# Kernel tuning notes

Hardware: AMD Instinct MI355X
Metric: run time of the kernel (lower is better)

The kernel has to match this reference:

```python
import jax, jax.numpy as jnp
import numpy as np

NUM_CLASSES = 80
STRIDES = (8, 16, 32)
RADIUS = 2.5
BOX_WEIGHT = 5.0
BIG = 1e9  # emulates restriction of cost/matching to union-candidate anchors
CAND_K = 10


def setup_inputs() -> dict:
    key = jax.random.key(0)
    ks = jax.random.split(key, 6)
    B, G = 16, 16
    p0 = jax.random.normal(ks[0], (B, NUM_CLASSES + 5, 160, 160), jnp.float32)
    p1 = jax.random.normal(ks[1], (B, NUM_CLASSES + 5, 80, 80), jnp.float32)
    p2 = jax.random.normal(ks[2], (B, NUM_CLASSES + 5, 40, 40), jnp.float32)
    cxy = jax.random.uniform(ks[3], (B, G, 2), jnp.float32, 64.0, 1216.0)
    wh = jax.random.uniform(ks[4], (B, G, 2), jnp.float32, 16.0, 256.0)
    cls = jax.random.randint(ks[5], (B, G, 1), 0, NUM_CLASSES).astype(jnp.float32)
    labels = jnp.concatenate([cxy, wh, cls], axis=-1)  # [B,G,5] xywh + class id
    return {"p0": p0, "p1": p1, "p2": p2, "labels": labels}


def _decode(p, stride):
    # [B,C,H,W] -> [B,HW,C] with xy=(xy+grid)*stride, wh=exp(wh)*stride
    B, C, H, W = p.shape
    out = jnp.transpose(p.reshape(B, C, H * W), (0, 2, 1))
    yy, xx = jnp.meshgrid(jnp.arange(H, dtype=p.dtype), jnp.arange(W, dtype=p.dtype), indexing='ij')
    gx, gy = xx.reshape(-1), yy.reshape(-1)
    xy = (out[..., :2] + jnp.stack([gx, gy], axis=-1)) * stride
    wh = jnp.exp(out[..., 2:4]) * stride
    return jnp.concatenate([xy, wh, out[..., 4:]], axis=-1), gx, gy


def _pair_iou(a, b):
    # a:[G,4], b:[A,4] in xywh -> [G,A]
    a1, a2 = a[:, :2] - a[:, 2:] * 0.5, a[:, :2] + a[:, 2:] * 0.5
    b1, b2 = b[:, :2] - b[:, 2:] * 0.5, b[:, :2] + b[:, 2:] * 0.5
    tl = jnp.maximum(a1[:, None], b1[None])
    br = jnp.minimum(a2[:, None], b2[None])
    wh = jnp.maximum(br - tl, 0.0)
    inter = wh[..., 0] * wh[..., 1]
    return inter / (a[:, 2] * a[:, 3])[:, None].__add__((b[:, 2] * b[:, 3])[None]).__sub__(inter).__add__(1e-16)


def _elem_iou(a, b):
    # elementwise xywh iou on [...,4]
    a1, a2 = a[..., :2] - a[..., 2:] * 0.5, a[..., :2] + a[..., 2:] * 0.5
    b1, b2 = b[..., :2] - b[..., 2:] * 0.5, b[..., :2] + b[..., 2:] * 0.5
    wh = jnp.maximum(jnp.minimum(a2, b2) - jnp.maximum(a1, b1), 0.0)
    inter = wh[..., 0] * wh[..., 1]
    return inter / (a[..., 2] * a[..., 3] + b[..., 2] * b[..., 3] - inter + 1e-16)


def _bce_logits(x, t):
    return jnp.maximum(x, 0.0) - x * t + jnp.log1p(jnp.exp(-jnp.abs(x)))


def _assign(tb, tc, pbox, pcls_l, pconf_l, xc, yc, sv):
    # Per-image SimOTA. tb:[G,4] tc:[G] pbox:[A,4] pcls_l:[A,C] pconf_l:[A]
    G = tb.shape[0]
    bx, by, bw, bh = tb[:, 0:1], tb[:, 1:2], tb[:, 2:3], tb[:, 3:4]
    in_box = (xc[None] > bx - bw * 0.5) & (xc[None] < bx + bw * 0.5) & \
             (yc[None] > by - bh * 0.5) & (yc[None] < by + bh * 0.5)  # [G,A]
    r = RADIUS * sv[None]
    in_mir = (xc[None] > bx - r) & (xc[None] < bx + r) & (yc[None] > by - r) & (yc[None] < by + r)
    union = jnp.any(in_box, 0) | jnp.any(in_mir, 0)  # [A]
    inter = in_box & in_mir  # [G,A]
    iou = _pair_iou(tb, pbox)  # [G,A]
    # cls cost: BCE(sqrt(sigmoid(cls)*sigmoid(conf)), one_hot) summed over classes
    p = jnp.sqrt(jax.nn.sigmoid(pcls_l) * jax.nn.sigmoid(pconf_l)[:, None])  # [A,C]
    logp = jnp.clip(jnp.log(p), -100.0, None)
    log1mp = jnp.clip(jnp.log1p(-p), -100.0, None)
    base = -log1mp.sum(-1)  # [A] = sum_c -log(1-p)
    cls_cost = base[None] - logp[:, tc].T + log1mp[:, tc].T  # [G,A]
    cost = cls_cost - 3.0 * jnp.log(iou + 1e-8) + 1e5 * (~inter) + BIG * (~union)[None]
    iou_m = jnp.where(union[None], iou, 0.0)
    dyn_k = jnp.maximum(jax.lax.top_k(iou_m, CAND_K)[0].sum(1).astype(jnp.int32), 1)  # [G]
    _, idx = jax.lax.top_k(-cost, CAND_K)  # per-gt lowest-cost anchors, sorted
    sel = (jnp.arange(CAND_K)[None] < dyn_k[:, None]).astype(cost.dtype)  # [G,K]
    matching = jnp.zeros_like(cost).at[jnp.arange(G)[:, None], idx].max(sel)  # [G,A]
    conflict = matching.sum(0) > 1.0
    gt_min = jnp.argmin(cost, axis=0)  # [A]
    onehot_min = (jnp.arange(G)[:, None] == gt_min[None]).astype(cost.dtype)
    matching = jnp.where(conflict[None], onehot_min, matching)
    fg = matching.sum(0) > 0.0  # [A]
    gidx = jnp.argmax(matching, axis=0)  # [A]
    miou = (matching * iou).sum(0)  # [A]
    t_cls = jax.nn.one_hot(tc[gidx], NUM_CLASSES, dtype=cost.dtype) * miou[:, None]  # [A,C]
    t_box = tb[gidx]  # [A,4]
    return fg, t_cls, t_box


def _forward(p0, p1, p2, labels):
    outs, xcs, ycs, svs = [], [], [], []
    for p, s in zip((p0, p1, p2), STRIDES):
        o, gx, gy = _decode(p, float(s))
        outs.append(o)
        xcs.append((gx + 0.5) * s)
        ycs.append((gy + 0.5) * s)
        svs.append(jnp.full_like(gx, s))
    out = jnp.concatenate(outs, axis=1)  # [B,A,85]
    xc, yc, sv = jnp.concatenate(xcs), jnp.concatenate(ycs), jnp.concatenate(svs)
    pbox, pconf, pcls = out[..., :4], out[..., 4], out[..., 5:]
    tb, tc = labels[..., :4], labels[..., 4].astype(jnp.int32)
    assign = jax.vmap(_assign, in_axes=(0, 0, 0, 0, 0, None, None, None))
    fg, t_cls, t_box = jax.lax.stop_gradient(assign(tb, tc, pbox, pcls, pconf, xc, yc, sv))
    fgf = fg.astype(pbox.dtype)  # target_conf == final fg mask
    loss_box = (fgf * (1.0 - _elem_iou(pbox, t_box) ** 2)).sum()
    loss_conf = _bce_logits(pconf, fgf).sum()
    loss_cls = (fgf[..., None] * _bce_logits(pcls, t_cls)).sum()
    fg_num = jnp.maximum(fgf.sum(), 1.0)
    return (BOX_WEIGHT * loss_box + loss_conf + loss_cls) / fg_num


def reference(p0, p1, p2, labels):
    return _forward(p0, p1, p2, labels)
```

## Files before the change

kernel.cpp:

```cpp
#include <hip/hip_runtime.h>
#include <hip/hip_bf16.h>
#include <cstdint>

#define NCLS 80
#define GNUM 16
#define BNUM 16
#define A0   25600
#define A1   6400
#define A2   1600
#define ATOT 33600
#define QTOT 16800
#define NBLK_A 132
#define NBLK_TOTAL (NBLK_A*BNUM)
#define NSPLIT 8
#define SEG   4200
#define WSEG  1050
#define NWAVE 32
#define FINF  3.4e38f
#define IINF  0x7fffffff

__device__ __forceinline__ float rcpf(float x){ return __builtin_amdgcn_rcpf(x); }
__device__ __forceinline__ float sqf (float x){ return __builtin_amdgcn_sqrtf(x); }
__device__ __forceinline__ float rsqf(float x){ return __builtin_amdgcn_rsqf(x); }

__device__ __forceinline__ float bce(float x, float t){
  float e = __expf(-fabsf(x));
  return fmaxf(x,0.f) - x*t + __logf(1.f + e);
}

__device__ __forceinline__ void get_level(const float* p0, const float* p1, const float* p2,
                                          int a, const float*& p, int& hw, int& off, int& W, float& s)
{
  if (a < A0){ p=p0; hw=A0; off=a; W=160; s=8.f; }
  else if (a < A0+A1){ p=p1; hw=A1; off=a-A0; W=80; s=16.f; }
  else { p=p2; hw=A2; off=a-A0-A1; W=40; s=32.f; }
}

__global__ __launch_bounds__(256, 8) void decode_cost_kernel(
    const float* __restrict__ p0, const float* __restrict__ p1, const float* __restrict__ p2,
    const float* __restrict__ labels,
    float* __restrict__ cost, float4* __restrict__ pbox, float* __restrict__ pconf,
    unsigned char* __restrict__ unionm)
{
  const int b = blockIdx.y;
  const int t = threadIdx.x;
  __shared__ float s_tb[GNUM][4];
  __shared__ int   s_tc[GNUM];
  if (t < GNUM){
    const float* L = labels + ((size_t)b*GNUM + t)*5;
    s_tb[t][0]=L[0]; s_tb[t][1]=L[1]; s_tb[t][2]=L[2]; s_tb[t][3]=L[3];
    s_tc[t]=(int)L[4];
  }
  __syncthreads();
  const int q = blockIdx.x*64 + (t>>2);
  const int k = t & 3;
  if (q >= QTOT) return;
  const int a0 = q*2;

  const float* p; int hw, off, W; float s;
  get_level(p0,p1,p2,a0,p,hw,off,W,s);
  const float* bp = p + (size_t)b*(NCLS+5)*hw + off;
  const float* cp = bp + 5*(size_t)hw;

  const float2 RX = *(const float2*)(bp);
  const float2 RY = *(const float2*)(bp + (size_t)hw);
  const float2 RW = *(const float2*)(bp + 2*(size_t)hw);
  const float2 RH = *(const float2*)(bp + 3*(size_t)hw);
  const float2 CL = *(const float2*)(bp + 4*(size_t)hw);

  int gx0 = off % W, gy0 = off / W;
  int gx1 = gx0+1, gy1 = gy0; if (gx1 >= W){ gx1 = 0; gy1++; }

  const float sc0 = rcpf(1.f + __expf(-CL.x));
  const float sc1 = rcpf(1.f + __expf(-CL.y));
  const float ssc0 = sqf(sc0),   ssc1 = sqf(sc1);
  const float rssc0 = rcpf(ssc0), rssc1 = rcpf(ssc1);

  float part0 = 0.f, part1 = 0.f;
  const int cb = 20*k;
  {
    float2 xv[8];
    #pragma unroll
    for (int j=0;j<8;j++) xv[j] = *(const float2*)(cp + (size_t)(cb+j)*hw);
    float pr0=1.f, pr1=1.f;
    #pragma unroll
    for (int j=0;j<8;j++){
      pr0 *= (1.f - ssc0*rsqf(1.f+__expf(-xv[j].x)));
      pr1 *= (1.f - ssc1*rsqf(1.f+__expf(-xv[j].y)));
    }
    part0 -= __logf(pr0); part1 -= __logf(pr1);
  }
  {
    float2 xv[8];
    #pragma unroll
    for (int j=0;j<8;j++) xv[j] = *(const float2*)(cp + (size_t)(cb+8+j)*hw);
    float pr0=1.f, pr1=1.f;
    #pragma unroll
    for (int j=0;j<8;j++){
      pr0 *= (1.f - ssc0*rsqf(1.f+__expf(-xv[j].x)));
      pr1 *= (1.f - ssc1*rsqf(1.f+__expf(-xv[j].y)));
    }
    part0 -= __logf(pr0); part1 -= __logf(pr1);
  }
  {
    float2 xv[4];
    #pragma unroll
    for (int j=0;j<4;j++) xv[j] = *(const float2*)(cp + (size_t)(cb+16+j)*hw);
    float pr0=1.f, pr1=1.f;
    #pragma unroll
    for (int j=0;j<4;j++){
      pr0 *= (1.f - ssc0*rsqf(1.f+__expf(-xv[j].x)));
      pr1 *= (1.f - ssc1*rsqf(1.f+__expf(-xv[j].y)));
    }
    part0 -= __logf(pr0); part1 -= __logf(pr1);
  }
  float base0 = part0 + __shfl_xor(part0, 1); base0 += __shfl_xor(base0, 2);
  float base1 = part1 + __shfl_xor(part1, 1); base1 += __shfl_xor(base1, 2);

  const float px0=(RX.x+gx0)*s, py0=(RY.x+gy0)*s, pw0=__expf(RW.x)*s, ph0=__expf(RH.x)*s;
  const float px1=(RX.y+gx1)*s, py1=(RY.y+gy1)*s, pw1=__expf(RW.y)*s, ph1=__expf(RH.y)*s;
  const float xc0=(gx0+0.5f)*s, yc0=(gy0+0.5f)*s;
  const float xc1=(gx1+0.5f)*s, yc1=(gy1+0.5f)*s;
  const float q1x0=px0-pw0*0.5f, q2x0=px0+pw0*0.5f, q1y0=py0-ph0*0.5f, q2y0=py0+ph0*0.5f;
  const float q1x1=px1-pw1*0.5f, q2x1=px1+pw1*0.5f, q1y1=py1-ph1*0.5f, q2y1=py1+ph1*0.5f;
  const float areaP0 = pw0*ph0, areaP1 = pw1*ph1;
  const float r = 2.5f*s;

  int mybits = 0;
  #pragma unroll
  for (int j=0;j<4;j++){
    const int g = k*4 + j;
    const float bx=s_tb[g][0], by=s_tb[g][1], bw=s_tb[g][2], bh=s_tb[g][3];
    const float b1x=bx-bw*0.5f, b2x=bx+bw*0.5f, b1y=by-bh*0.5f, b2y=by+bh*0.5f;
    const bool u0 = ((xc0>b1x)&&(xc0<b2x)&&(yc0>b1y)&&(yc0<b2y))
                  || ((xc0>bx-r)&&(xc0<bx+r)&&(yc0>by-r)&&(yc0<by+r));
    const bool u1 = ((xc1>b1x)&&(xc1<b2x)&&(yc1>b1y)&&(yc1<b2y))
                  || ((xc1>bx-r)&&(xc1<bx+r)&&(yc1>by-r)&&(yc1<by+r));
    mybits |= (u0?1:0) | (u1?2:0);
  }
  mybits |= __shfl_xor(mybits, 1);
  mybits |= __shfl_xor(mybits, 2);
  const float add0 = (mybits&1)?0.f:1e9f, add1 = (mybits&2)?0.f:1e9f;

  const size_t rowb = (size_t)b*GNUM*ATOT + a0;

  #pragma unroll
  for (int j=0;j<4;j++){
    const int g = k*4 + j;
    const float2 x = *(const float2*)(cp + (size_t)s_tc[g]*hw);
    const float e0 = __expf(-x.x), e1 = __expf(-x.y);
    const float rp0 = rssc0*sqf(1.f+e0), rp1 = rssc1*sqf(1.f+e1);
    const float cd0 = __logf(fmaxf(rp0-1.f, 1e-30f));
    const float cd1 = __logf(fmaxf(rp1-1.f, 1e-30f));

    const float bx=s_tb[g][0], by=s_tb[g][1], bw=s_tb[g][2], bh=s_tb[g][3];
    const float b1x=bx-bw*0.5f, b2x=bx+bw*0.5f, b1y=by-bh*0.5f, b2y=by+bh*0.5f;
    const float areaB = bw*bh;

    const bool inb0 = (xc0>b1x)&&(xc0<b2x)&&(yc0>b1y)&&(yc0<b2y);
    const bool inm0 = (xc0>bx-r)&&(xc0<bx+r)&&(yc0>by-r)&&(yc0<by+r);
    const bool inb1 = (xc1>b1x)&&(xc1<b2x)&&(yc1>b1y)&&(yc1<b2y);
    const bool inm1 = (xc1>bx-r)&&(xc1<bx+r)&&(yc1>by-r)&&(yc1<by+r);

    float iw,ih,inte;
    iw = fmaxf(fminf(b2x,q2x0)-fmaxf(b1x,q1x0),0.f);
    ih = fmaxf(fminf(b2y,q2y0)-fmaxf(b1y,q1y0),0.f);
    inte = iw*ih;
    const float iou0 = inte * rcpf(areaB+areaP0-inte+1e-16f);
    iw = fmaxf(fminf(b2x,q2x1)-fmaxf(b1x,q1x1),0.f);
    ih = fmaxf(fminf(b2y,q2y1)-fmaxf(b1y,q1y1),0.f);
    inte = iw*ih;
    const float iou1 = inte * rcpf(areaB+areaP1-inte+1e-16f);

    float2 cst;
    cst.x = base0 + cd0 - 3.f*__logf(iou0+1e-8f) + ((inb0&&inm0)?0.f:100000.f) + add0;
    cst.y = base1 + cd1 - 3.f*__logf(iou1+1e-8f) + ((inb1&&inm1)?0.f:100000.f) + add1;
    *(float2*)(cost + rowb + (size_t)g*ATOT) = cst;
  }

  if (k == 0){
    pbox[(size_t)b*ATOT+a0  ] = make_float4(px0,py0,pw0,ph0);
    pbox[(size_t)b*ATOT+a0+1] = make_float4(px1,py1,pw1,ph1);
    *(float2*)(pconf + (size_t)b*ATOT + a0) = make_float2(CL.x, CL.y);
    uchar2 um; um.x = (mybits&1)?1:0; um.y = (mybits&2)?1:0;
    *(uchar2*)(unionm + (size_t)b*ATOT + a0) = um;
  }
}

__global__ __launch_bounds__(256) void topk_stage1(
    const float* __restrict__ cost, const float4* __restrict__ pbox,
    const unsigned char* __restrict__ unionm, const float* __restrict__ labels,
    float* __restrict__ cand_c, int* __restrict__ cand_i, float* __restrict__ cand_v)
{
  const int bg   = blockIdx.y;
  const int b    = bg >> 4;
  const int seg  = blockIdx.x;
  const int wave = threadIdx.x >> 6;
  const int lane = threadIdx.x & 63;
  const int wg   = seg*4 + wave;

  const float*  crow = cost + (size_t)bg*ATOT;
  const float4* prow = pbox + (size_t)b*ATOT;
  const unsigned char* urow = unionm + (size_t)b*ATOT;
  const float bx = labels[bg*5+0], by = labels[bg*5+1];
  const float bw = labels[bg*5+2], bh = labels[bg*5+3];
  const float areaB = bw*bh;
  const float b1x=bx-bw*0.5f, b2x=bx+bw*0.5f, b1y=by-bh*0.5f, b2y=by+bh*0.5f;

  const int start = seg*SEG + wave*WSEG;
  const int end   = start + WSEG;

  float cv[10]; int ci[10]; float iv[10];
  #pragma unroll
  for (int k=0;k<10;k++){ cv[k]=FINF; ci[k]=IINF; iv[k]=0.f; }

  for (int a = start + lane; a < end; a += 64){
    float c = crow[a];
    if (c < cv[9] || (c == cv[9] && a < ci[9])){
      float nc=c; int ni=a;
      #pragma unroll
      for (int k=0;k<10;k++){
        bool better = (nc < cv[k]) || (nc==cv[k] && ni<ci[k]);
        float tv=cv[k]; int ti=ci[k];
        cv[k]=better?nc:cv[k]; ci[k]=better?ni:ci[k];
        nc  =better?tv:nc;     ni  =better?ti:ni;
      }
    }
    if (urow[a]){
      float4 pb = prow[a];
      float tlx=fmaxf(b1x, pb.x-pb.z*0.5f), brx=fminf(b2x, pb.x+pb.z*0.5f);
      float tly=fmaxf(b1y, pb.y-pb.w*0.5f), bry=fminf(b2y, pb.y+pb.w*0.5f);
      float iw=fmaxf(brx-tlx,0.f), ih=fmaxf(bry-tly,0.f);
      float inte=iw*ih;
      float io = inte * rcpf(areaB + pb.z*pb.w - inte + 1e-16f);
      if (io > iv[9]){
        float nv=io;
        #pragma unroll
        for (int k=0;k<10;k++){
          bool better = nv > iv[k];
          float tv=iv[k];
          iv[k]=better?nv:iv[k];
          nv  =better?tv:nv;
        }
      }
    }
  }

  float selc = 0.f; int seli = 0;
  #pragma unroll
  for (int r=0;r<10;r++){
    float bv = cv[0]; int bi = ci[0];
    #pragma unroll
    for (int off=32; off>0; off>>=1){
      float ov = __shfl_xor(bv, off);
      int   oi = __shfl_xor(bi, off);
      bool take = (ov < bv) || (ov==bv && oi<bi);
      bv = take?ov:bv; bi = take?oi:bi;
    }
    if (lane == r){ selc = bv; seli = bi; }
    if (cv[0]==bv && ci[0]==bi){
      #pragma unroll
      for (int k=0;k<9;k++){ cv[k]=cv[k+1]; ci[k]=ci[k+1]; }
      cv[9]=FINF; ci[9]=IINF;
    }
  }
  float selv = 0.f;
  #pragma unroll
  for (int r=0;r<10;r++){
    float bv = iv[0]; int bl = lane;
    #pragma unroll
    for (int off=32; off>0; off>>=1){
      float ov = __shfl_xor(bv, off);
      int   ol = __shfl_xor(bl, off);
      bool take = (ov > bv) || (ov==bv && ol<bl);
      bv = take?ov:bv; bl = take?ol:bl;
    }
    if (lane == r) selv = bv;
    if (lane == bl){
      #pragma unroll
      for (int k=0;k<9;k++){ iv[k]=iv[k+1]; }
      iv[9]=0.f;
    }
  }

  if (lane < 10){
    const size_t base = ((size_t)bg*NWAVE + wg)*10 + lane;
    cand_c[base] = selc;
    cand_i[base] = seli;
    cand_v[base] = selv;
  }
}

__global__ __launch_bounds__(64) void topk_stage2(
    const float* __restrict__ cand_c, const int* __restrict__ cand_i,
    const float* __restrict__ cand_v, unsigned int* __restrict__ match_mask)
{
  const int bg = blockIdx.x;
  const int b = bg >> 4, g = bg & 15;
  const int lane = threadIdx.x;
  const size_t base = (size_t)bg*NWAVE*10 + lane*5;

  float cv[5]; int ci[5]; float iv[5];
  #pragma unroll
  for (int k=0;k<5;k++){ cv[k]=cand_c[base+k]; ci[k]=cand_i[base+k]; iv[k]=cand_v[base+k]; }

  int seli = 0;
  #pragma unroll
  for (int r=0;r<10;r++){
    float bv = cv[0]; int bi = ci[0];
    #pragma unroll
    for (int off=32; off>0; off>>=1){
      float ov = __shfl_xor(bv, off);
      int   oi = __shfl_xor(bi, off);
      bool take = (ov < bv) || (ov==bv && oi<bi);
      bv = take?ov:bv; bi = take?oi:bi;
    }
    if (lane == r) seli = bi;
    if (cv[0]==bv && ci[0]==bi){
      #pragma unroll
      for (int k=0;k<4;k++){ cv[k]=cv[k+1]; ci[k]=ci[k+1]; }
      cv[4]=FINF; ci[4]=IINF;
    }
  }

  float isum = 0.f;
  #pragma unroll
  for (int r=0;r<10;r++){
    float bv = iv[0]; int bl = lane;
    #pragma unroll
    for (int off=32; off>0; off>>=1){
      float ov = __shfl_xor(bv, off);
      int   ol = __shfl_xor(bl, off);
      bool take = (ov > bv) || (ov==bv && ol<bl);
      bv = take?ov:bv; bl = take?ol:bl;
    }
    isum += bv;
    if (lane == bl){
      #pragma unroll
      for (int k=0;k<4;k++){ iv[k]=iv[k+1]; }
      iv[4]=0.f;
    }
  }

  int dynk = (int)isum;
  if (dynk < 1)  dynk = 1;
  if (dynk > 10) dynk = 10;
  if (lane < dynk)
    atomicOr(&match_mask[(size_t)b*ATOT + seli], 1u<<g);
}

__global__ __launch_bounds__(256) void loss_kernel(
    const float* __restrict__ p0, const float* __restrict__ p1, const float* __restrict__ p2,
    const float* __restrict__ labels,
    const float* __restrict__ cost, const float4* __restrict__ pbox,
    const float* __restrict__ pconf, const unsigned int* __restrict__ match_mask,
    float* __restrict__ blocksums)
{
  const int b = blockIdx.y;
  const int a = blockIdx.x*256 + threadIdx.x;
  float lbox=0.f, lconf=0.f, lcls=0.f, fgn=0.f;
  if (a < ATOT){
    unsigned int m = match_mask[(size_t)b*ATOT+a];
    float cl = pconf[(size_t)b*ATOT+a];
    if (m != 0u){
      int gidx;
      if (__popc(m) > 1){
        float best = FINF; int bgi = 0;
        for (int g=0; g<GNUM; g++){
          float c = cost[((size_t)b*GNUM+g)*ATOT + a];
          if (c < best){ best=c; bgi=g; }
        }
        gidx = bgi;
      } else {
        gidx = __ffs(m)-1;
      }
      const float* L = labels + ((size_t)b*GNUM+gidx)*5;
      float bx=L[0], by=L[1], bw=L[2], bh=L[3];
      int tcg=(int)L[4];
      float4 pb = pbox[(size_t)b*ATOT+a];
      float tlx=fmaxf(bx-bw*0.5f, pb.x-pb.z*0.5f);
      float brx=fminf(bx+bw*0.5f, pb.x+pb.z*0.5f);
      float tly=fmaxf(by-bh*0.5f, pb.y-pb.w*0.5f);
      float bry=fminf(by+bh*0.5f, pb.y+pb.w*0.5f);
      float iw=fmaxf(brx-tlx,0.f), ih=fmaxf(bry-tly,0.f);
      float inte=iw*ih;
      float iou = inte * rcpf(bw*bh + pb.z*pb.w - inte + 1e-16f);
      lbox = 1.f - iou*iou;
      lconf = bce(cl, 1.f);
      float miou = iou;
      const float* p; int hw, off, W; float s;
      get_level(p0,p1,p2,a,p,hw,off,W,s);
      const float* bp = p + (size_t)b*(NCLS+5)*hw + off;
      for (int c=0;c<NCLS;c++){
        float x = bp[(size_t)(5+c)*hw];
        float t = (c==tcg)? miou : 0.f;
        lcls += bce(x, t);
      }
      fgn = 1.f;
    } else {
      lconf = bce(cl, 0.f);
    }
  }
  #pragma unroll
  for (int off2=32; off2>0; off2>>=1){
    lbox  += __shfl_down(lbox,  off2);
    lconf += __shfl_down(lconf, off2);
    lcls  += __shfl_down(lcls,  off2);
    fgn   += __shfl_down(fgn,   off2);
  }
  __shared__ float s_red[4][4];
  const int wave = threadIdx.x >> 6;
  if ((threadIdx.x & 63)==0){
    s_red[wave][0]=lbox; s_red[wave][1]=lconf; s_red[wave][2]=lcls; s_red[wave][3]=fgn;
  }
  __syncthreads();
  if (threadIdx.x==0){
    float r0=0,r1=0,r2=0,r3=0;
    #pragma unroll
    for (int w=0;w<4;w++){ r0+=s_red[w][0]; r1+=s_red[w][1]; r2+=s_red[w][2]; r3+=s_red[w][3]; }
    const int bid = blockIdx.y*gridDim.x + blockIdx.x;
    ((float4*)blocksums)[bid] = make_float4(r0,r1,r2,r3);
  }
}

__global__ __launch_bounds__(256) void finalize_kernel(
    const float* __restrict__ blocksums, float* __restrict__ out)
{
  const int tid = threadIdx.x;
  float r0=0,r1=0,r2=0,r3=0;
  for (int i = tid; i < NBLK_TOTAL; i += 256){
    const float4 v = ((const float4*)blocksums)[i];
    r0+=v.x; r1+=v.y; r2+=v.z; r3+=v.w;
  }
  #pragma unroll
  for (int off=32; off>0; off>>=1){
    r0 += __shfl_down(r0, off);
    r1 += __shfl_down(r1, off);
    r2 += __shfl_down(r2, off);
    r3 += __shfl_down(r3, off);
  }
  __shared__ float s_red[4][4];
  const int wave = tid >> 6;
  if ((tid & 63)==0){ s_red[wave][0]=r0; s_red[wave][1]=r1; s_red[wave][2]=r2; s_red[wave][3]=r3; }
  __syncthreads();
  if (tid==0){
    float t0=0,t1=0,t2=0,t3=0;
    #pragma unroll
    for (int w=0;w<4;w++){ t0+=s_red[w][0]; t1+=s_red[w][1]; t2+=s_red[w][2]; t3+=s_red[w][3]; }
    out[0] = (5.f*t0 + t1 + t2) / fmaxf(t3, 1.f);
  }
}

extern "C" void kernel_launch(void* const* d_in, const int* in_sizes, int n_in,
                              void* d_out, int out_size, void* d_ws, size_t ws_size,
                              hipStream_t stream)
{
  const float* p0     = (const float*)d_in[0];
  const float* p1     = (const float*)d_in[1];
  const float* p2     = (const float*)d_in[2];
  const float* labels = (const float*)d_in[3];

  char* ws = (char*)d_ws;
  size_t o = 0;
  float*        cost       = (float*)(ws + o);        o += (size_t)BNUM*GNUM*ATOT*4;
  float4*       pbox       = (float4*)(ws + o);       o += (size_t)BNUM*ATOT*16;
  float*        pconf      = (float*)(ws + o);        o += (size_t)BNUM*ATOT*4;
  unsigned int* match_mask = (unsigned int*)(ws + o); o += (size_t)BNUM*ATOT*4;
  unsigned char* unionm    = (unsigned char*)(ws + o);o += (size_t)BNUM*ATOT;
  o = (o + 255) & ~(size_t)255;
  float*        blocksums  = (float*)(ws + o);        o += (size_t)NBLK_TOTAL*4*4;
  o = (o + 255) & ~(size_t)255;
  float*        cand_c     = (float*)(ws + o);        o += (size_t)256*NWAVE*10*4;
  int*          cand_i     = (int*)(ws + o);          o += (size_t)256*NWAVE*10*4;
  float*        cand_v     = (float*)(ws + o);        o += (size_t)256*NWAVE*10*4;

  hipMemsetAsync(match_mask, 0, (size_t)BNUM*ATOT*4, stream);

  dim3 gridA((QTOT + 63)/64, BNUM);
  decode_cost_kernel<<<gridA, 256, 0, stream>>>(p0,p1,p2,labels,cost,pbox,pconf,unionm);
  dim3 gridT(NSPLIT, BNUM*GNUM);
  topk_stage1<<<gridT, 256, 0, stream>>>(cost, pbox, unionm, labels, cand_c, cand_i, cand_v);
  topk_stage2<<<BNUM*GNUM, 64, 0, stream>>>(cand_c, cand_i, cand_v, match_mask);
  dim3 gridC(NBLK_A, BNUM);
  loss_kernel<<<gridC, 256, 0, stream>>>(p0,p1,p2,labels,cost,pbox,pconf,match_mask,blocksums);
  finalize_kernel<<<1, 256, 0, stream>>>(blocksums, (float*)d_out);
}
```

Baseline: 142.7 us.

## Fuse per-block top-k into decode kernel and drop global cost matrix

The decode kernel now keeps each block's 16x128 cost and IoU tiles in shared memory and does a wave-level top-10 selection there, writing only small candidate lists instead of the full B*G*A cost matrix. A merge kernel reduces these candidates, and the loss kernel recomputes cost for multi-matched anchors instead of reading the stored matrix. This removes roughly 34 MB of cost writes and reads and the separate memset, since match_mask is zeroed inside the decode kernel. In exchange it adds in-kernel reduction work, extra shared memory (lower occupancy), and redundant class reads for conflicting anchors.

```diff
diff --git a/kernel.cpp b/kernel.cpp
--- a/kernel.cpp
+++ b/kernel.cpp
@@ -12,9 +12,9 @@
 #define QTOT 16800
 #define NBLK_A 132
 #define NBLK_TOTAL (NBLK_A*BNUM)
-#define NSPLIT 8
-#define SEG   4200
-#define WSEG  1050
+#define NSEG 263
+#define NC   (NSEG*10)
+#define CHUNK 83
 #define NWAVE 32
 #define FINF  3.4e38f
 #define IINF  0x7fffffff
@@ -39,185 +39,237 @@
 __global__ __launch_bounds__(256, 8) void decode_cost_kernel(
     const float* __restrict__ p0, const float* __restrict__ p1, const float* __restrict__ p2,
     const float* __restrict__ labels,
-    float* __restrict__ cost, float4* __restrict__ pbox, float* __restrict__ pconf,
-    unsigned char* __restrict__ unionm)
+    float4* __restrict__ pbox, float* __restrict__ pconf,
+    unsigned char* __restrict__ unionm, unsigned int* __restrict__ match_mask,
+    float* __restrict__ cand1_c, int* __restrict__ cand1_i, float* __restrict__ cand1_v)
 {
   const int b = blockIdx.y;
   const int t = threadIdx.x;
   __shared__ float s_tb[GNUM][4];
   __shared__ int   s_tc[GNUM];
+  __shared__ float s_cost[GNUM][128];
+  __shared__ float s_iou [GNUM][128];
   if (t < GNUM){
     const float* L = labels + ((size_t)b*GNUM + t)*5;
     s_tb[t][0]=L[0]; s_tb[t][1]=L[1]; s_tb[t][2]=L[2]; s_tb[t][3]=L[3];
     s_tc[t]=(int)L[4];
   }
   __syncthreads();
-  const int q = blockIdx.x*64 + (t>>2);
+  const int p_loc = t>>2;
+  const int q = blockIdx.x*64 + p_loc;
   const int k = t & 3;
-  if (q >= QTOT) return;
-  const int a0 = q*2;
-
-  const float* p; int hw, off, W; float s;
-  get_level(p0,p1,p2,a0,p,hw,off,W,s);
-  const float* bp = p + (size_t)b*(NCLS+5)*hw + off;
-  const float* cp = bp + 5*(size_t)hw;
-
-  const float2 RX = *(const float2*)(bp);
-  const float2 RY = *(const float2*)(bp + (size_t)hw);
-  const float2 RW = *(const float2*)(bp + 2*(size_t)hw);
-  const float2 RH = *(const float2*)(bp + 3*(size_t)hw);
-  const float2 CL = *(const float2*)(bp + 4*(size_t)hw);
-
-  int gx0 = off % W, gy0 = off / W;
-  int gx1 = gx0+1, gy1 = gy0; if (gx1 >= W){ gx1 = 0; gy1++; }
-
-  const float sc0 = rcpf(1.f + __expf(-CL.x));
-  const float sc1 = rcpf(1.f + __expf(-CL.y));
-  const float ssc0 = sqf(sc0),   ssc1 = sqf(sc1);
-  const float rssc0 = rcpf(ssc0), rssc1 = rcpf(ssc1);
-
-  float part0 = 0.f, part1 = 0.f;
-  const int cb = 20*k;
-  {
-    float2 xv[8];
-    #pragma unroll
-    for (int j=0;j<8;j++) xv[j] = *(const float2*)(cp + (size_t)(cb+j)*hw);
-    float pr0=1.f, pr1=1.f;
-    #pragma unroll
-    for (int j=0;j<8;j++){
-      pr0 *= (1.f - ssc0*rsqf(1.f+__expf(-xv[j].x)));
-      pr1 *= (1.f - ssc1*rsqf(1.f+__expf(-xv[j].y)));
-    }
-    part0 -= __logf(pr0); part1 -= __logf(pr1);
-  }
-  {
-    float2 xv[8];
-    #pragma unroll
-    for (int j=0;j<8;j++) xv[j] = *(const float2*)(cp + (size_t)(cb+8+j)*hw);
-    float pr0=1.f, pr1=1.f;
-    #pragma unroll
-    for (int j=0;j<8;j++){
-      pr0 *= (1.f - ssc0*rsqf(1.f+__expf(-xv[j].x)));
-      pr1 *= (1.f - ssc1*rsqf(1.f+__expf(-xv[j].y)));
-    }
-    part0 -= __logf(pr0); part1 -= __logf(pr1);
-  }
-  {
-    float2 xv[4];
-    #pragma unroll
-    for (int j=0;j<4;j++) xv[j] = *(const float2*)(cp + (size_t)(cb+16+j)*hw);
-    float pr0=1.f, pr1=1.f;
+  const bool valid = (q < QTOT);
+
+  if (!valid){
     #pragma unroll
     for (int j=0;j<4;j++){
-      pr0 *= (1.f - ssc0*rsqf(1.f+__expf(-xv[j].x)));
-      pr1 *= (1.f - ssc1*rsqf(1.f+__expf(-xv[j].y)));
-    }
-    part0 -= __logf(pr0); part1 -= __logf(pr1);
-  }
-  float base0 = part0 + __shfl_xor(part0, 1); base0 += __shfl_xor(base0, 2);
-  float base1 = part1 + __shfl_xor(part1, 1); base1 += __shfl_xor(base1, 2);
-
-  const float px0=(RX.x+gx0)*s, py0=(RY.x+gy0)*s, pw0=__expf(RW.x)*s, ph0=__expf(RH.x)*s;
-  const float px1=(RX.y+gx1)*s, py1=(RY.y+gy1)*s, pw1=__expf(RW.y)*s, ph1=__expf(RH.y)*s;
-  const float xc0=(gx0+0.5f)*s, yc0=(gy0+0.5f)*s;
-  const float xc1=(gx1+0.5f)*s, yc1=(gy1+0.5f)*s;
-  const float q1x0=px0-pw0*0.5f, q2x0=px0+pw0*0.5f, q1y0=py0-ph0*0.5f, q2y0=py0+ph0*0.5f;
-  const float q1x1=px1-pw1*0.5f, q2x1=px1+pw1*0.5f, q1y1=py1-ph1*0.5f, q2y1=py1+ph1*0.5f;
-  const float areaP0 = pw0*ph0, areaP1 = pw1*ph1;
-  const float r = 2.5f*s;
-
-  int mybits = 0;
-  #pragma unroll
-  for (int j=0;j<4;j++){
-    const int g = k*4 + j;
-    const float bx=s_tb[g][0], by=s_tb[g][1], bw=s_tb[g][2], bh=s_tb[g][3];
-    const float b1x=bx-bw*0.5f, b2x=bx+bw*0.5f, b1y=by-bh*0.5f, b2y=by+bh*0.5f;
-    const bool u0 = ((xc0>b1x)&&(xc0<b2x)&&(yc0>b1y)&&(yc0<b2y))
-                  || ((xc0>bx-r)&&(xc0<bx+r)&&(yc0>by-r)&&(yc0<by+r));
-    const bool u1 = ((xc1>b1x)&&(xc1<b2x)&&(yc1>b1y)&&(yc1<b2y))
-                  || ((xc1>bx-r)&&(xc1<bx+r)&&(yc1>by-r)&&(yc1<by+r));
-    mybits |= (u0?1:0) | (u1?2:0);
-  }
-  mybits |= __shfl_xor(mybits, 1);
-  mybits |= __shfl_xor(mybits, 2);
-  const float add0 = (mybits&1)?0.f:1e9f, add1 = (mybits&2)?0.f:1e9f;
-
-  const size_t rowb = (size_t)b*GNUM*ATOT + a0;
-
-  #pragma unroll
-  for (int j=0;j<4;j++){
-    const int g = k*4 + j;
-    const float2 x = *(const float2*)(cp + (size_t)s_tc[g]*hw);
-    const float e0 = __expf(-x.x), e1 = __expf(-x.y);
-    const float rp0 = rssc0*sqf(1.f+e0), rp1 = rssc1*sqf(1.f+e1);
-    const float cd0 = __logf(fmaxf(rp0-1.f, 1e-30f));
-    const float cd1 = __logf(fmaxf(rp1-1.f, 1e-30f));
-
-    const float bx=s_tb[g][0], by=s_tb[g][1], bw=s_tb[g][2], bh=s_tb[g][3];
-    const float b1x=bx-bw*0.5f, b2x=bx+bw*0.5f, b1y=by-bh*0.5f, b2y=by+bh*0.5f;
-    const float areaB = bw*bh;
-
-    const bool inb0 = (xc0>b1x)&&(xc0<b2x)&&(yc0>b1y)&&(yc0<b2y);
-    const bool inm0 = (xc0>bx-r)&&(xc0<bx+r)&&(yc0>by-r)&&(yc0<by+r);
-    const bool inb1 = (xc1>b1x)&&(xc1<b2x)&&(yc1>b1y)&&(yc1<b2y);
-    const bool inm1 = (xc1>bx-r)&&(xc1<bx+r)&&(yc1>by-r)&&(yc1<by+r);
-
-    float iw,ih,inte;
-    iw = fmaxf(fminf(b2x,q2x0)-fmaxf(b1x,q1x0),0.f);
-    ih = fmaxf(fminf(b2y,q2y0)-fmaxf(b1y,q1y0),0.f);
-    inte = iw*ih;
-    const float iou0 = inte * rcpf(areaB+areaP0-inte+1e-16f);
-    iw = fmaxf(fminf(b2x,q2x1)-fmaxf(b1x,q1x1),0.f);
-    ih = fmaxf(fminf(b2y,q2y1)-fmaxf(b1y,q1y1),0.f);
-    inte = iw*ih;
-    const float iou1 = inte * rcpf(areaB+areaP1-inte+1e-16f);
-
-    float2 cst;
-    cst.x = base0 + cd0 - 3.f*__logf(iou0+1e-8f) + ((inb0&&inm0)?0.f:100000.f) + add0;
-    cst.y = base1 + cd1 - 3.f*__logf(iou1+1e-8f) + ((inb1&&inm1)?0.f:100000.f) + add1;
-    *(float2*)(cost + rowb + (size_t)g*ATOT) = cst;
-  }
-
-  if (k == 0){
-    pbox[(size_t)b*ATOT+a0  ] = make_float4(px0,py0,pw0,ph0);
-    pbox[(size_t)b*ATOT+a0+1] = make_float4(px1,py1,pw1,ph1);
-    *(float2*)(pconf + (size_t)b*ATOT + a0) = make_float2(CL.x, CL.y);
-    uchar2 um; um.x = (mybits&1)?1:0; um.y = (mybits&2)?1:0;
-    *(uchar2*)(unionm + (size_t)b*ATOT + a0) = um;
-  }
-}
-
-__global__ __launch_bounds__(256) void topk_stage1(
-    const float* __restrict__ cost, const float4* __restrict__ pbox,
-    const unsigned char* __restrict__ unionm, const float* __restrict__ labels,
+      const int g = k*4 + j;
+      s_cost[g][2*p_loc]   = FINF;  s_cost[g][2*p_loc+1] = FINF;
+      s_iou [g][2*p_loc]   = 0.f;   s_iou [g][2*p_loc+1] = 0.f;
+    }
+  } else {
+    const int a0 = q*2;
+    const float* p; int hw, off, W; float s;
+    get_level(p0,p1,p2,a0,p,hw,off,W,s);
+    const float* bp = p + (size_t)b*(NCLS+5)*hw + off;
+    const float* cp = bp + 5*(size_t)hw;
+
+    const float2 RX = *(const float2*)(bp);
+    const float2 RY = *(const float2*)(bp + (size_t)hw);
+    const float2 RW = *(const float2*)(bp + 2*(size_t)hw);
+    const float2 RH = *(const float2*)(bp + 3*(size_t)hw);
+    const float2 CL = *(const float2*)(bp + 4*(size_t)hw);
+
+    int gx0 = off % W, gy0 = off / W;
+    int gx1 = gx0+1, gy1 = gy0; if (gx1 >= W){ gx1 = 0; gy1++; }
+
+    const float sc0 = rcpf(1.f + __expf(-CL.x));
+    const float sc1 = rcpf(1.f + __expf(-CL.y));
+    const float ssc0 = sqf(sc0),   ssc1 = sqf(sc1);
+    const float rssc0 = rcpf(ssc0), rssc1 = rcpf(ssc1);
+
+    float part0 = 0.f, part1 = 0.f;
+    const int cb = 20*k;
+    {
+      float2 xv[8];
+      #pragma unroll
+      for (int j=0;j<8;j++) xv[j] = *(const float2*)(cp + (size_t)(cb+j)*hw);
+      float pr0=1.f, pr1=1.f;
+      #pragma unroll
+      for (int j=0;j<8;j++){
+        pr0 *= (1.f - ssc0*rsqf(1.f+__expf(-xv[j].x)));
+        pr1 *= (1.f - ssc1*rsqf(1.f+__expf(-xv[j].y)));
+      }
+      part0 -= __logf(pr0); part1 -= __logf(pr1);
+    }
+    {
+      float2 xv[8];
+      #pragma unroll
+      for (int j=0;j<8;j++) xv[j] = *(const float2*)(cp + (size_t)(cb+8+j)*hw);
+      float pr0=1.f, pr1=1.f;
+      #pragma unroll
+      for (int j=0;j<8;j++){
+        pr0 *= (1.f - ssc0*rsqf(1.f+__expf(-xv[j].x)));
+        pr1 *= (1.f - ssc1*rsqf(1.f+__expf(-xv[j].y)));
+      }
+      part0 -= __logf(pr0); part1 -= __logf(pr1);
+    }
+    {
+      float2 xv[4];
+      #pragma unroll
+      for (int j=0;j<4;j++) xv[j] = *(const float2*)(cp + (size_t)(cb+16+j)*hw);
+      float pr0=1.f, pr1=1.f;
+      #pragma unroll
+      for (int j=0;j<4;j++){
+        pr0 *= (1.f - ssc0*rsqf(1.f+__expf(-xv[j].x)));
+        pr1 *= (1.f - ssc1*rsqf(1.f+__expf(-xv[j].y)));
+      }
+      part0 -= __logf(pr0); part1 -= __logf(pr1);
+    }
+    float base0 = part0 + __shfl_xor(part0, 1); base0 += __shfl_xor(base0, 2);
+    float base1 = part1 + __shfl_xor(part1, 1); base1 += __shfl_xor(base1, 2);
+
+    const float px0=(RX.x+gx0)*s, py0=(RY.x+gy0)*s, pw0=__expf(RW.x)*s, ph0=__expf(RH.x)*s;
+    const float px1=(RX.y+gx1)*s, py1=(RY.y+gy1)*s, pw1=__expf(RW.y)*s, ph1=__expf(RH.y)*s;
+    const float xc0=(gx0+0.5f)*s, yc0=(gy0+0.5f)*s;
+    const float xc1=(gx1+0.5f)*s, yc1=(gy1+0.5f)*s;
+    const float q1x0=px0-pw0*0.5f, q2x0=px0+pw0*0.5f, q1y0=py0-ph0*0.5f, q2y0=py0+ph0*0.5f;
+    const float q1x1=px1-pw1*0.5f, q2x1=px1+pw1*0.5f, q1y1=py1-ph1*0.5f, q2y1=py1+ph1*0.5f;
+    const float areaP0 = pw0*ph0, areaP1 = pw1*ph1;
+    const float r = 2.5f*s;
+
+    int mybits = 0;
+    #pragma unroll
+    for (int j=0;j<4;j++){
+      const int g = k*4 + j;
+      const float bx=s_tb[g][0], by=s_tb[g][1], bw=s_tb[g][2], bh=s_tb[g][3];
+      const float b1x=bx-bw*0.5f, b2x=bx+bw*0.5f, b1y=by-bh*0.5f, b2y=by+bh*0.5f;
+      const bool u0 = ((xc0>b1x)&&(xc0<b2x)&&(yc0>b1y)&&(yc0<b2y))
+                    || ((xc0>bx-r)&&(xc0<bx+r)&&(yc0>by-r)&&(yc0<by+r));
+      const bool u1 = ((xc1>b1x)&&(xc1<b2x)&&(yc1>b1y)&&(yc1<b2y))
+                    || ((xc1>bx-r)&&(xc1<bx+r)&&(yc1>by-r)&&(yc1<by+r));
+      mybits |= (u0?1:0) | (u1?2:0);
+    }
+    mybits |= __shfl_xor(mybits, 1);
+    mybits |= __shfl_xor(mybits, 2);
+    const float add0 = (mybits&1)?0.f:1e9f, add1 = (mybits&2)?0.f:1e9f;
+
+    #pragma unroll
+    for (int j=0;j<4;j++){
+      const int g = k*4 + j;
+      const float2 x = *(const float2*)(cp + (size_t)s_tc[g]*hw);
+      const float e0 = __expf(-x.x), e1 = __expf(-x.y);
+      const float rp0 = rssc0*sqf(1.f+e0), rp1 = rssc1*sqf(1.f+e1);
+      const float cd0 = __logf(fmaxf(rp0-1.f, 1e-30f));
+      const float cd1 = __logf(fmaxf(rp1-1.f, 1e-30f));
+
+      const float bx=s_tb[g][0], by=s_tb[g][1], bw=s_tb[g][2], bh=s_tb[g][3];
+      const float b1x=bx-bw*0.5f, b2x=bx+bw*0.5f, b1y=by-bh*0.5f, b2y=by+bh*0.5f;
+      const float areaB = bw*bh;
+
+      const bool inb0 = (xc0>b1x)&&(xc0<b2x)&&(yc0>b1y)&&(yc0<b2y);
+      const bool inm0 = (xc0>bx-r)&&(xc0<bx+r)&&(yc0>by-r)&&(yc0<by+r);
+      const bool inb1 = (xc1>b1x)&&(xc1<b2x)&&(yc1>b1y)&&(yc1<b2y);
+      const bool inm1 = (xc1>bx-r)&&(xc1<bx+r)&&(yc1>by-r)&&(yc1<by+r);
+
+      float iw,ih,inte;
+      iw = fmaxf(fminf(b2x,q2x0)-fmaxf(b1x,q1x0),0.f);
+      ih = fmaxf(fminf(b2y,q2y0)-fmaxf(b1y,q1y0),0.f);
+      inte = iw*ih;
+      const float iou0 = inte * rcpf(areaB+areaP0-inte+1e-16f);
+      iw = fmaxf(fminf(b2x,q2x1)-fmaxf(b1x,q1x1),0.f);
+      ih = fmaxf(fminf(b2y,q2y1)-fmaxf(b1y,q1y1),0.f);
+      inte = iw*ih;
+      const float iou1 = inte * rcpf(areaB+areaP1-inte+1e-16f);
+
+      s_cost[g][2*p_loc]   = base0 + cd0 - 3.f*__logf(iou0+1e-8f) + ((inb0&&inm0)?0.f:100000.f) + add0;
+      s_cost[g][2*p_loc+1] = base1 + cd1 - 3.f*__logf(iou1+1e-8f) + ((inb1&&inm1)?0.f:100000.f) + add1;
+      s_iou [g][2*p_loc]   = (mybits&1)? iou0 : 0.f;
+      s_iou [g][2*p_loc+1] = (mybits&2)? iou1 : 0.f;
+    }
+
+    if (k == 0){
+      const int a0w = q*2;
+      pbox[(size_t)b*ATOT+a0w  ] = make_float4(px0,py0,pw0,ph0);
+      pbox[(size_t)b*ATOT+a0w+1] = make_float4(px1,py1,pw1,ph1);
+      *(float2*)(pconf + (size_t)b*ATOT + a0w) = make_float2(CL.x, CL.y);
+      uchar2 um; um.x = (mybits&1)?1:0; um.y = (mybits&2)?1:0;
+      *(uchar2*)(unionm + (size_t)b*ATOT + a0w) = um;
+      uint2 z; z.x=0u; z.y=0u;
+      *(uint2*)(match_mask + (size_t)b*ATOT + a0w) = z;
+    }
+  }
+  __syncthreads();
+
+  const int wave = t>>6, lane = t&63;
+  #pragma unroll
+  for (int gg=0; gg<4; gg++){
+    const int g = wave*4 + gg;
+    const size_t cbase = ((size_t)(b*GNUM+g)*NSEG + blockIdx.x)*10;
+
+    float c0 = s_cost[g][lane],    c1 = s_cost[g][lane+64];
+    int   i0 = blockIdx.x*128+lane, i1 = blockIdx.x*128+lane+64;
+    {
+      bool sw = (c1 < c0) || (c1==c0 && i1 < i0);
+      float tc=c0; int ti=i0;
+      c0 = sw?c1:c0; i0 = sw?i1:i0;
+      c1 = sw?tc:c1; i1 = sw?ti:i1;
+    }
+    float selc=0.f; int seli=0;
+    #pragma unroll
+    for (int r2=0;r2<10;r2++){
+      float bv=c0; int bi=i0;
+      #pragma unroll
+      for (int off=32; off>0; off>>=1){
+        float ov=__shfl_xor(bv,off); int oi=__shfl_xor(bi,off);
+        bool take=(ov<bv)||(ov==bv&&oi<bi);
+        bv=take?ov:bv; bi=take?oi:bi;
+      }
+      if (lane==r2){ selc=bv; seli=bi; }
+      if (c0==bv && i0==bi){ c0=c1; i0=i1; c1=FINF; i1=IINF; }
+    }
+    if (lane<10){ cand1_c[cbase+lane]=selc; cand1_i[cbase+lane]=seli; }
+
+    float v0 = s_iou[g][lane], v1 = s_iou[g][lane+64];
+    if (v1 > v0){ float tv=v0; v0=v1; v1=tv; }
+    float selv=0.f;
+    #pragma unroll
+    for (int r2=0;r2<10;r2++){
+      float bv=v0; int bl=lane;
+      #pragma unroll
+      for (int off=32; off>0; off>>=1){
+        float ov=__shfl_xor(bv,off); int ol=__shfl_xor(bl,off);
+        bool take=(ov>bv)||(ov==bv&&ol<bl);
+        bv=take?ov:bv; bl=take?ol:bl;
+      }
+      if (lane==r2) selv=bv;
+      if (lane==bl){ v0=v1; v1=0.f; }
+    }
+    if (lane<10) cand1_v[cbase+lane]=selv;
+  }
+}
+
+__global__ __launch_bounds__(256) void topk_merge1(
+    const float* __restrict__ cand1_c, const int* __restrict__ cand1_i,
+    const float* __restrict__ cand1_v,
     float* __restrict__ cand_c, int* __restrict__ cand_i, float* __restrict__ cand_v)
 {
   const int bg   = blockIdx.y;
-  const int b    = bg >> 4;
-  const int seg  = blockIdx.x;
   const int wave = threadIdx.x >> 6;
   const int lane = threadIdx.x & 63;
-  const int wg   = seg*4 + wave;
-
-  const float*  crow = cost + (size_t)bg*ATOT;
-  const float4* prow = pbox + (size_t)b*ATOT;
-  const unsigned char* urow = unionm + (size_t)b*ATOT;
-  const float bx = labels[bg*5+0], by = labels[bg*5+1];
-  const float bw = labels[bg*5+2], bh = labels[bg*5+3];
-  const float areaB = bw*bh;
-  const float b1x=bx-bw*0.5f, b2x=bx+bw*0.5f, b1y=by-bh*0.5f, b2y=by+bh*0.5f;
-
-  const int start = seg*SEG + wave*WSEG;
-  const int end   = start + WSEG;
+  const int wg   = blockIdx.x*4 + wave;
+  const size_t base1 = (size_t)bg*NC;
+  const int start = wg*CHUNK;
+  const int end   = (start+CHUNK < NC)? start+CHUNK : NC;
 
   float cv[10]; int ci[10]; float iv[10];
   #pragma unroll
   for (int k=0;k<10;k++){ cv[k]=FINF; ci[k]=IINF; iv[k]=0.f; }
 
-  for (int a = start + lane; a < end; a += 64){
-    float c = crow[a];
-    if (c < cv[9] || (c == cv[9] && a < ci[9])){
-      float nc=c; int ni=a;
+  for (int c = start + lane; c < end; c += 64){
+    float cc = cand1_c[base1+c]; int ii = cand1_i[base1+c];
+    if (cc < cv[9] || (cc == cv[9] && ii < ci[9])){
+      float nc=cc; int ni=ii;
       #pragma unroll
       for (int k=0;k<10;k++){
         bool better = (nc < cv[k]) || (nc==cv[k] && ni<ci[k]);
@@ -226,22 +278,15 @@
         nc  =better?tv:nc;     ni  =better?ti:ni;
       }
     }
-    if (urow[a]){
-      float4 pb = prow[a];
-      float tlx=fmaxf(b1x, pb.x-pb.z*0.5f), brx=fminf(b2x, pb.x+pb.z*0.5f);
-      float tly=fmaxf(b1y, pb.y-pb.w*0.5f), bry=fminf(b2y, pb.y+pb.w*0.5f);
-      float iw=fmaxf(brx-tlx,0.f), ih=fmaxf(bry-tly,0.f);
-      float inte=iw*ih;
-      float io = inte * rcpf(areaB + pb.z*pb.w - inte + 1e-16f);
-      if (io > iv[9]){
-        float nv=io;
-        #pragma unroll
-        for (int k=0;k<10;k++){
-          bool better = nv > iv[k];
-          float tv=iv[k];
-          iv[k]=better?nv:iv[k];
-          nv  =better?tv:nv;
-        }
+    float vv = cand1_v[base1+c];
+    if (vv > iv[9]){
+      float nv=vv;
+      #pragma unroll
+      for (int k=0;k<10;k++){
+        bool better = nv > iv[k];
+        float tv=iv[k];
+        iv[k]=better?nv:iv[k];
+        nv  =better?tv:nv;
       }
     }
   }
@@ -352,8 +397,8 @@
 __global__ __launch_bounds__(256) void loss_kernel(
     const float* __restrict__ p0, const float* __restrict__ p1, const float* __restrict__ p2,
     const float* __restrict__ labels,
-    const float* __restrict__ cost, const float4* __restrict__ pbox,
-    const float* __restrict__ pconf, const unsigned int* __restrict__ match_mask,
+    const float4* __restrict__ pbox, const float* __restrict__ pconf,
+    const unsigned char* __restrict__ unionm, const unsigned int* __restrict__ match_mask,
     float* __restrict__ blocksums)
 {
   const int b = blockIdx.y;
@@ -363,12 +408,60 @@
     unsigned int m = match_mask[(size_t)b*ATOT+a];
     float cl = pconf[(size_t)b*ATOT+a];
     if (m != 0u){
+      const float* p; int hw, off, W; float s;
+      get_level(p0,p1,p2,a,p,hw,off,W,s);
+      const float* bp = p + (size_t)b*(NCLS+5)*hw + off;
+      const float* cp = bp + 5*(size_t)hw;
       int gidx;
       if (__popc(m) > 1){
+        float sc = rcpf(1.f + __expf(-cl));
+        float ssc = sqf(sc); float rssc = rcpf(ssc);
+        float part[4];
+        #pragma unroll
+        for (int kk=0; kk<4; kk++){
+          const int cb2 = 20*kk;
+          float pk = 0.f, pr;
+          pr = 1.f;
+          #pragma unroll
+          for (int j=0;j<8;j++)  pr *= (1.f - ssc*rsqf(1.f+__expf(-cp[(size_t)(cb2+j)*hw])));
+          pk -= __logf(pr);
+          pr = 1.f;
+          #pragma unroll
+          for (int j=8;j<16;j++) pr *= (1.f - ssc*rsqf(1.f+__expf(-cp[(size_t)(cb2+j)*hw])));
+          pk -= __logf(pr);
+          pr = 1.f;
+          #pragma unroll
+          for (int j=16;j<20;j++)pr *= (1.f - ssc*rsqf(1.f+__expf(-cp[(size_t)(cb2+j)*hw])));
+          pk -= __logf(pr);
+          part[kk] = pk;
+        }
+        const float base = (part[0]+part[1])+(part[2]+part[3]);
+        const int gx = off % W, gy = off / W;
+        const float xc=(gx+0.5f)*s, yc=(gy+0.5f)*s, r=2.5f*s;
+        const float4 pb = pbox[(size_t)b*ATOT+a];
+        const float q1x=pb.x-pb.z*0.5f, q2x=pb.x+pb.z*0.5f;
+        const float q1y=pb.y-pb.w*0.5f, q2y=pb.y+pb.w*0.5f;
+        const float areaP = pb.z*pb.w;
+        const float addu = unionm[(size_t)b*ATOT+a] ? 0.f : 1e9f;
         float best = FINF; int bgi = 0;
         for (int g=0; g<GNUM; g++){
-          float c = cost[((size_t)b*GNUM+g)*ATOT + a];
-          if (c < best){ best=c; bgi=g; }
+          const float* L = labels + ((size_t)b*GNUM+g)*5;
+          const float bx=L[0], by=L[1], bw=L[2], bh=L[3];
+          const int tc=(int)L[4];
+          const float x = cp[(size_t)tc*hw];
+          const float e = __expf(-x);
+          const float rp = rssc*sqf(1.f+e);
+          const float cd = __logf(fmaxf(rp-1.f, 1e-30f));
+          const float b1x=bx-bw*0.5f, b2x=bx+bw*0.5f, b1y=by-bh*0.5f, b2y=by+bh*0.5f;
+          const float areaB = bw*bh;
+          const bool inb = (xc>b1x)&&(xc<b2x)&&(yc>b1y)&&(yc<b2y);
+          const bool inm = (xc>bx-r)&&(xc<bx+r)&&(yc>by-r)&&(yc<by+r);
+          float iw = fmaxf(fminf(b2x,q2x)-fmaxf(b1x,q1x),0.f);
+          float ih = fmaxf(fminf(b2y,q2y)-fmaxf(b1y,q1y),0.f);
+          float inte = iw*ih;
+          const float iou = inte * rcpf(areaB+areaP-inte+1e-16f);
+          const float cg = base + cd - 3.f*__logf(iou+1e-8f) + ((inb&&inm)?0.f:100000.f) + addu;
+          if (cg < best){ best=cg; bgi=g; }
         }
         gidx = bgi;
       } else {
@@ -388,11 +481,8 @@
       lbox = 1.f - iou*iou;
       lconf = bce(cl, 1.f);
       float miou = iou;
-      const float* p; int hw, off, W; float s;
-      get_level(p0,p1,p2,a,p,hw,off,W,s);
-      const float* bp = p + (size_t)b*(NCLS+5)*hw + off;
       for (int c=0;c<NCLS;c++){
-        float x = bp[(size_t)(5+c)*hw];
+        float x = cp[(size_t)c*hw];
         float t = (c==tcg)? miou : 0.f;
         lcls += bce(x, t);
       }
@@ -462,7 +552,6 @@
 
   char* ws = (char*)d_ws;
   size_t o = 0;
-  float*        cost       = (float*)(ws + o);        o += (size_t)BNUM*GNUM*ATOT*4;
   float4*       pbox       = (float4*)(ws + o);       o += (size_t)BNUM*ATOT*16;
   float*        pconf      = (float*)(ws + o);        o += (size_t)BNUM*ATOT*4;
   unsigned int* match_mask = (unsigned int*)(ws + o); o += (size_t)BNUM*ATOT*4;
@@ -470,18 +559,21 @@
   o = (o + 255) & ~(size_t)255;
   float*        blocksums  = (float*)(ws + o);        o += (size_t)NBLK_TOTAL*4*4;
   o = (o + 255) & ~(size_t)255;
+  float*        cand1_c    = (float*)(ws + o);        o += (size_t)256*NC*4;
+  int*          cand1_i    = (int*)(ws + o);          o += (size_t)256*NC*4;
+  float*        cand1_v    = (float*)(ws + o);        o += (size_t)256*NC*4;
+  o = (o + 255) & ~(size_t)255;
   float*        cand_c     = (float*)(ws + o);        o += (size_t)256*NWAVE*10*4;
   int*          cand_i     = (int*)(ws + o);          o += (size_t)256*NWAVE*10*4;
   float*        cand_v     = (float*)(ws + o);        o += (size_t)256*NWAVE*10*4;
 
-  hipMemsetAsync(match_mask, 0, (size_t)BNUM*ATOT*4, stream);
-
-  dim3 gridA((QTOT + 63)/64, BNUM);
-  decode_cost_kernel<<<gridA, 256, 0, stream>>>(p0,p1,p2,labels,cost,pbox,pconf,unionm);
-  dim3 gridT(NSPLIT, BNUM*GNUM);
-  topk_stage1<<<gridT, 256, 0, stream>>>(cost, pbox, unionm, labels, cand_c, cand_i, cand_v);
+  dim3 gridA(NSEG, BNUM);
+  decode_cost_kernel<<<gridA, 256, 0, stream>>>(p0,p1,p2,labels,pbox,pconf,unionm,match_mask,
+                                                cand1_c,cand1_i,cand1_v);
+  dim3 gridM(8, BNUM*GNUM);
+  topk_merge1<<<gridM, 256, 0, stream>>>(cand1_c,cand1_i,cand1_v,cand_c,cand_i,cand_v);
   topk_stage2<<<BNUM*GNUM, 64, 0, stream>>>(cand_c, cand_i, cand_v, match_mask);
   dim3 gridC(NBLK_A, BNUM);
-  loss_kernel<<<gridC, 256, 0, stream>>>(p0,p1,p2,labels,cost,pbox,pconf,match_mask,blocksums);
+  loss_kernel<<<gridC, 256, 0, stream>>>(p0,p1,p2,labels,pbox,pconf,unionm,match_mask,blocksums);
   finalize_kernel<<<1, 256, 0, stream>>>(blocksums, (float*)d_out);
 }
```

Result: slower. 270.8 us (+89.8%).
